# Kernel optimization log

Hardware: AMD Instinct MI355X
Metric: run time of the kernel (lower is better)

## Reference

```python
import jax, jax.numpy as jnp
import numpy as np

TOP_K = 128
HID = 256


def _mlp2(h, w1, b1, w2, b2):
    return jax.nn.relu(h @ w1 + b1) @ w2 + b2


def setup_inputs() -> dict:
    key = jax.random.key(0)
    ks = jax.random.split(key, 20)
    B, L, D = 512, 256, 64
    s = 0.05
    inp = {
        "x": jax.random.normal(ks[0], (B, L, D), dtype=jnp.float32),
        "Wq": jax.random.normal(ks[1], (D, HID)) * s, "bq": jnp.zeros((HID,)),
        "Wk": jax.random.normal(ks[2], (D, HID)) * s, "bk": jnp.zeros((HID,)),
        "phi_w1": jax.random.normal(ks[3], (D, HID)) * s, "phi_b1": jnp.zeros((HID,)),
        "phi_w2": jax.random.normal(ks[4], (HID, HID)) * s, "phi_b2": jnp.zeros((HID,)),
        "xi_w1": jax.random.normal(ks[5], (2 * D, HID)) * s, "xi_b1": jnp.zeros((HID,)),
        "xi_w2": jax.random.normal(ks[6], (HID, HID)) * s, "xi_b2": jnp.zeros((HID,)),
        "rho_w1": jax.random.normal(ks[7], (HID, HID)) * s, "rho_b1": jnp.zeros((HID,)),
        "rho_w2": jax.random.normal(ks[8], (HID, 128)) * s, "rho_b2": jnp.zeros((128,)),
    }
    return inp


def reference(x, Wq, bq, Wk, bk, phi_w1, phi_b1, phi_w2, phi_b2,
              xi_w1, xi_b1, xi_w2, xi_b2, rho_w1, rho_b1, rho_w2, rho_b2):
    B, L, D = x.shape
    scale = HID ** (-0.5)
    # padding mask (all True for randn input; trim is identity with static shapes)
    pad = jnp.sum(jnp.abs(x), axis=-1) != 0  # [B, L]
    Q = x @ Wq + bq  # [B, L, H]
    K = x @ Wk + bk
    scores = jnp.einsum("blh,bmh->blm", Q, K) * scale  # [B, L, L]
    mask2d = pad[:, :, None] & pad[:, None, :]
    scores = jnp.where(mask2d, scores, -jnp.inf)
    flat = scores.reshape(B, L * L)
    k = min(TOP_K, L * L)
    topk_vals, topk_idx = jax.lax.top_k(flat, k)  # [B, k]
    topk_w = jax.nn.softmax(topk_vals, axis=-1)
    row = topk_idx // L
    col = topk_idx % L
    x_i = jnp.take_along_axis(x, row[:, :, None], axis=1)  # [B, k, D]
    x_j = jnp.take_along_axis(x, col[:, :, None], axis=1)
    feat_self = _mlp2(x_i, phi_w1, phi_b1, phi_w2, phi_b2)  # [B, k, H]
    feat_pair = _mlp2(jnp.concatenate([x_i, x_j], axis=-1), xi_w1, xi_b1, xi_w2, xi_b2)
    self_mask = (row == col)[:, :, None]
    interaction = jnp.where(self_mask, feat_self, feat_pair)
    pooled = jnp.sum(interaction * topk_w[:, :, None], axis=1)  # [B, H]
    return _mlp2(pooled, rho_w1, rho_b1, rho_w2, rho_b2)  # [B, 128]
```

## Files before the change

### kernel.cpp

```cpp
#include <hip/hip_runtime.h>

typedef unsigned short u16;
typedef unsigned int   u32;
typedef unsigned char  u8;
typedef unsigned long long u64;

#define B_TOT 512
#define L_SEQ 256
#define D_IN  64
#define HIDN  256
#define TOPK  128
#define CAP   160
#define NWT   32
#define FLDS  76304

typedef float  f32x4  __attribute__((ext_vector_type(4)));
typedef __bf16 bf16x8 __attribute__((ext_vector_type(8)));

__device__ __forceinline__ u16 f2bf(float f){
  u32 u = __float_as_uint(f);
  u32 r = u + 0x7fffu + ((u>>16)&1u);
  return (u16)(r>>16);
}
__device__ __forceinline__ u32 sortKey(float f){
  u32 b = __float_as_uint(f);
  return (b & 0x80000000u) ? ~b : (b | 0x80000000u);
}
__device__ __forceinline__ float unKey(u32 u){
  u32 b = (u & 0x80000000u) ? (u & 0x7fffffffu) : ~u;
  return __uint_as_float(b);
}
__device__ __forceinline__ void cvt8(const float* v, u32* hp, u32* lp){
  #pragma unroll
  for (int i=0;i<4;++i){
    float v0 = v[2*i], v1 = v[2*i+1];
    u16 h0 = f2bf(v0); float h0f = __uint_as_float(((u32)h0)<<16); u16 l0 = f2bf(v0 - h0f);
    u16 h1 = f2bf(v1); float h1f = __uint_as_float(((u32)h1)<<16); u16 l1 = f2bf(v1 - h1f);
    hp[i] = (u32)h0 | ((u32)h1<<16);
    lp[i] = (u32)l0 | ((u32)l1<<16);
  }
}

__global__ __launch_bounds__(256) void k_wprep(
    const float* __restrict__ Wq, const float* __restrict__ bq,
    const float* __restrict__ Wk, const float* __restrict__ bk,
    const float* __restrict__ xi_w1, const float* __restrict__ phi_w1,
    u16* __restrict__ MtH, u16* __restrict__ MtL, float* __restrict__ uvc,
    u16* __restrict__ xiH, u16* __restrict__ xiL,
    u16* __restrict__ phiH, u16* __restrict__ phiL)
{
  int bid = blockIdx.x, tid = threadIdx.x;
  if (bid < 64){
    __shared__ float wq[HIDN];
    __shared__ float part[256];
    int a = bid;
    wq[tid] = Wq[a*HIDN + tid];
    __syncthreads();
    int bcol = tid & 63, q = tid >> 6;
    float s = 0.f;
    for (int h = q*64; h < q*64 + 64; ++h)
      s = fmaf(wq[h], Wk[bcol*HIDN + h], s);
    part[tid] = s;
    __syncthreads();
    if (tid < 64){
      float mv = part[tid] + part[64+tid] + part[128+tid] + part[192+tid];
      u16 hh = f2bf(mv); float hf = __uint_as_float(((u32)hh)<<16);
      u16 ll = f2bf(mv - hf);
      MtH[tid*64 + a] = hh;
      MtL[tid*64 + a] = ll;
    }
    int wv = tid >> 6, ln = tid & 63;
    if (wv == 0){
      float s2 = 0.f;
      #pragma unroll
      for (int i=0;i<4;++i){ int h = ln*4+i; s2 = fmaf(wq[h], bk[h], s2); }
      #pragma unroll
      for (int off=1; off<64; off<<=1) s2 += __shfl_xor(s2, off);
      if (ln == 0) uvc[a] = s2;
    } else if (wv == 1){
      float s2 = 0.f;
      #pragma unroll
      for (int i=0;i<4;++i){ int h = ln*4+i; s2 = fmaf(Wk[a*HIDN + h], bq[h], s2); }
      #pragma unroll
      for (int off=1; off<64; off<<=1) s2 += __shfl_xor(s2, off);
      if (ln == 0) uvc[64 + a] = s2;
    } else if (wv == 2 && a == 0){
      float s2 = 0.f;
      #pragma unroll
      for (int i=0;i<4;++i){ int h = ln*4+i; s2 = fmaf(bq[h], bk[h], s2); }
      #pragma unroll
      for (int off=1; off<64; off<<=1) s2 += __shfl_xor(s2, off);
      if (ln == 0) uvc[128] = s2;
    }
  } else {
    int t = (bid-64)*256 + tid;
    if (t < 256*128){
      int h = t >> 7, d = t & 127;
      float v = xi_w1[d*HIDN + h];
      u16 hh = f2bf(v); float hf = __uint_as_float(((u32)hh)<<16);
      u16 ll = f2bf(v - hf);
      xiH[h*128 + d] = hh; xiL[h*128 + d] = ll;
    } else {
      int t2 = t - 256*128;
      int h = t2 >> 6, d = t2 & 63;
      float v = phi_w1[d*HIDN + h];
      u16 hh = f2bf(v); float hf = __uint_as_float(((u32)hh)<<16);
      u16 ll = f2bf(v - hf);
      phiH[h*64 + d] = hh; phiL[h*64 + d] = ll;
    }
  }
}

__global__ __launch_bounds__(1024, 1) void k_fused(
    const float* __restrict__ x, const u16* __restrict__ MtH, const u16* __restrict__ MtL,
    const float* __restrict__ uvc,
    u64* __restrict__ cand, int* __restrict__ cand_n, u32* __restrict__ uthr)
{
  extern __shared__ __align__(16) u16 smem[];
  u16* XH = smem;
  u16* XL = XH + 256*72;
  float* STS = (float*)(XL + 256*72);
  float* STT = STS + 256;
  float* SUV = STT + 256;

  int tid = threadIdx.x;
  int b = blockIdx.x;
  const float* xb = x + (size_t)b*(L_SEQ*D_IN);

  if (tid < 129) SUV[tid] = uvc[tid];

  int ar = tid >> 2, aq = tid & 3;
  float v[16];
  {
    const float* src = xb + (size_t)ar*D_IN + aq*16;
    #pragma unroll
    for (int i=0;i<4;++i) *(float4*)&v[i*4] = *(const float4*)(src + i*4);
    u32 hpA[4],lpA[4],hpB[4],lpB[4];
    cvt8(&v[0], hpA, lpA); cvt8(&v[8], hpB, lpB);
    u16* dh = XH + ar*72 + aq*16;
    u16* dl = XL + ar*72 + aq*16;
    *(uint4*)(dh)     = make_uint4(hpA[0],hpA[1],hpA[2],hpA[3]);
    *(uint4*)(dh + 8) = make_uint4(hpB[0],hpB[1],hpB[2],hpB[3]);
    *(uint4*)(dl)     = make_uint4(lpA[0],lpA[1],lpA[2],lpA[3]);
    *(uint4*)(dl + 8) = make_uint4(lpB[0],lpB[1],lpB[2],lpB[3]);
  }
  __syncthreads();

  {
    float su=0.f, tv=0.f, pa=0.f;
    #pragma unroll
    for (int d=0; d<16; ++d){
      float xa = v[d];
      su = fmaf(xa, SUV[aq*16+d], su);
      tv = fmaf(xa, SUV[64+aq*16+d], tv);
      pa += fabsf(xa);
    }
    su += __shfl_xor(su,1); su += __shfl_xor(su,2);
    tv += __shfl_xor(tv,1); tv += __shfl_xor(tv,2);
    pa += __shfl_xor(pa,1); pa += __shfl_xor(pa,2);
    if (aq == 0){
      bool pad = (pa != 0.f);
      STS[ar] = pad ? (su + SUV[128]) : -1e38f;
      STT[ar] = pad ? tv : -1e38f;
    }
  }
  __syncthreads();

  int w = tid >> 6, lane = tid & 63, lm = lane & 15, quad = lane >> 4;
  int u  = w;
  int r0 = u*16;

  bf16x8 Yh0, Yh1, Yl0, Yl1;
  {
    const u16* xh_ = XH + (r0+lm)*72;
    const u16* xl_ = XL + (r0+lm)*72;
    bf16x8 Xh0 = *(const bf16x8*)(xh_ + quad*8);
    bf16x8 Xh1 = *(const bf16x8*)(xh_ + 32 + quad*8);
    bf16x8 Xl0 = *(const bf16x8*)(xl_ + quad*8);
    bf16x8 Xl1 = *(const bf16x8*)(xl_ + 32 + quad*8);
    u32 yh[8], yl[8];
    #pragma unroll
    for (int ct=0; ct<4; ++ct){
      int srow = 8*(lm>>2) + 4*(ct&1) + (lm&3) + 32*(ct>>1);
      const u16* mth = MtH + srow*64 + quad*8;
      const u16* mtl = MtL + srow*64 + quad*8;
      bf16x8 Mh0 = *(const bf16x8*)(mth);
      bf16x8 Mh1 = *(const bf16x8*)(mth + 32);
      bf16x8 Ml0 = *(const bf16x8*)(mtl);
      bf16x8 Ml1 = *(const bf16x8*)(mtl + 32);
      f32x4 a1 = {0.f,0.f,0.f,0.f}, a2 = {0.f,0.f,0.f,0.f};
      a1 = __builtin_amdgcn_mfma_f32_16x16x32_bf16(Mh0, Xh0, a1, 0,0,0);
      a2 = __builtin_amdgcn_mfma_f32_16x16x32_bf16(Mh1, Xh1, a2, 0,0,0);
      a1 = __builtin_amdgcn_mfma_f32_16x16x32_bf16(Ml0, Xh0, a1, 0,0,0);
      a2 = __builtin_amdgcn_mfma_f32_16x16x32_bf16(Ml1, Xh1, a2, 0,0,0);
      a1 = __builtin_amdgcn_mfma_f32_16x16x32_bf16(Mh0, Xl0, a1, 0,0,0);
      a2 = __builtin_amdgcn_mfma_f32_16x16x32_bf16(Mh1, Xl1, a2, 0,0,0);
      #pragma unroll
      for (int pr=0; pr<2; ++pr){
        float v0 = a1[2*pr]   + a2[2*pr];
        float v1 = a1[2*pr+1] + a2[2*pr+1];
        u16 h0 = f2bf(v0); u16 h1 = f2bf(v1);
        u16 l0 = f2bf(v0 - __uint_as_float(((u32)h0)<<16));
        u16 l1 = f2bf(v1 - __uint_as_float(((u32)h1)<<16));
        int slot = (ct>>1)*4 + (ct&1)*2 + pr;
        yh[slot] = (u32)h0 | ((u32)h1<<16);
        yl[slot] = (u32)l0 | ((u32)l1<<16);
      }
    }
    uint4 t0 = make_uint4(yh[0],yh[1],yh[2],yh[3]);
    uint4 t1 = make_uint4(yh[4],yh[5],yh[6],yh[7]);
    uint4 t2 = make_uint4(yl[0],yl[1],yl[2],yl[3]);
    uint4 t3 = make_uint4(yl[4],yl[5],yl[6],yl[7]);
    Yh0 = *(const bf16x8*)&t0;
    Yh1 = *(const bf16x8*)&t1;
    Yl0 = *(const bf16x8*)&t2;
    Yl1 = *(const bf16x8*)&t3;
  }

  float sr[4];
  #pragma unroll
  for (int r=0;r<4;++r) sr[r] = STS[r0 + quad*4 + r];

  for (int ch=0; ch<2; ++ch){
    int j0 = ch*128;
    u32 kv[32];
    #pragma unroll
    for (int ct=0; ct<8; ++ct){
      const u16* bh = XH + (j0 + ct*16+lm)*72;
      const u16* bl = XL + (j0 + ct*16+lm)*72;
      bf16x8 Bh0 = *(const bf16x8*)(bh + quad*8);
      bf16x8 Bh1 = *(const bf16x8*)(bh + 32 + quad*8);
      bf16x8 Bl0 = *(const bf16x8*)(bl + quad*8);
      bf16x8 Bl1 = *(const bf16x8*)(bl + 32 + quad*8);
      f32x4 a1 = {0.f,0.f,0.f,0.f}, a2 = {0.f,0.f,0.f,0.f};
      a1 = __builtin_amdgcn_mfma_f32_16x16x32_bf16(Yh0, Bh0, a1, 0,0,0);
      a2 = __builtin_amdgcn_mfma_f32_16x16x32_bf16(Yh1, Bh1, a2, 0,0,0);
      a1 = __builtin_amdgcn_mfma_f32_16x16x32_bf16(Yl0, Bh0, a1, 0,0,0);
      a2 = __builtin_amdgcn_mfma_f32_16x16x32_bf16(Yl1, Bh1, a2, 0,0,0);
      a1 = __builtin_amdgcn_mfma_f32_16x16x32_bf16(Yh0, Bl0, a1, 0,0,0);
      a2 = __builtin_amdgcn_mfma_f32_16x16x32_bf16(Yh1, Bl1, a2, 0,0,0);
      float tc = STT[j0 + ct*16 + lm];
      #pragma unroll
      for (int r=0;r<4;++r)
        kv[ct*4 + r] = sortKey(a1[r] + a2[r] + sr[r] + tc);
    }

    u32 T = 0;
    for (int bit=15; bit>=0; --bit){
      u32 th2 = (T | (1u<<bit)) << 16;
      int c0 = 0, c1 = 0;
      #pragma unroll
      for (int i=0;i<32;i+=2){
        c0 += (int)__popcll(__ballot(kv[i]   >= th2));
        c1 += (int)__popcll(__ballot(kv[i+1] >= th2));
      }
      int c = c0 + c1;
      if (c >= TOPK){
        T |= (1u<<bit);
        if (c <= CAP) break;
      }
    }
    u32 thr = T << 16;
    u32 up  = (T < 0xffffu) ? ((T+1u) << 16) : 0xffffffffu;

    u32 m1 = 0, m2 = 0;
    #pragma unroll
    for (int i=0;i<32;++i){
      bool ge = kv[i] >= thr;
      bool c1 = ge && (kv[i] >= up);
      m1 |= (c1 ? 1u : 0u) << i;
      m2 |= ((ge && !c1) ? 1u : 0u) << i;
    }
    int n1 = __popc(m1), n2 = __popc(m2);
    int p1 = n1, p2 = n2;
    #pragma unroll
    for (int off=1; off<64; off<<=1){
      int a = __shfl_up(p1, off); if (lane >= off) p1 += a;
      int c = __shfl_up(p2, off); if (lane >= off) p2 += c;
    }
    int tot1 = __shfl(p1, 63), tot2 = __shfl(p2, 63);
    int pos1 = p1 - n1;
    int pos2 = tot1 + (p2 - n2);
    int total = tot1 + tot2;
    int wt = u*2 + ch;
    size_t base = ((size_t)b*NWT + wt)*CAP;
    if (lane == 0){
      cand_n[b*NWT + wt] = (total < CAP) ? total : CAP;
      uthr[b*NWT + wt] = thr;
    }
    {
      int o1=0, o2=0;
      #pragma unroll
      for (int i=0;i<32;++i){
        bool c1 = (m1 >> i) & 1u, c2v = (m2 >> i) & 1u;
        if (c1 | c2v){
          int p = c1 ? (pos1 + o1) : (pos2 + o2);
          int flat = (r0 + quad*4 + (i&3))*L_SEQ + (j0 + (i>>2)*16 + lm);
          if (p < CAP) cand[base + p] = ((u64)kv[i] << 32) | (u32)flat;
        }
        o1 += c1; o2 += c2v;
      }
    }
  }
}

__global__ __launch_bounds__(256) void k_pre(
    const float* __restrict__ x, const u16* __restrict__ MtH, const u16* __restrict__ MtL,
    const float* __restrict__ uvc,
    u16* __restrict__ xh, u16* __restrict__ xl,
    u16* __restrict__ yh, u16* __restrict__ yl,
    float* __restrict__ st)
{
  __shared__ __align__(16) u16 sh[64][72];
  __shared__ __align__(16) u16 sl[64][72];
  __shared__ float sUV[132];
  int tid = threadIdx.x;
  int g0 = blockIdx.x * 64;
  int b  = g0 >> 8, l0 = g0 & 255;
  int r = tid >> 2, q = tid & 3;

  if (tid < 129) sUV[tid] = uvc[tid];

  float v[16];
  {
    const float* xr = x + (size_t)(g0 + r)*D_IN + q*16;
    #pragma unroll
    for (int i=0;i<4;++i) *(float4*)&v[i*4] = *(const float4*)(xr + i*4);
  }
  {
    u32 hpA[4],lpA[4],hpB[4],lpB[4];
    cvt8(&v[0], hpA, lpA); cvt8(&v[8], hpB, lpB);
    size_t xo = (size_t)(g0 + r)*D_IN + q*16;
    *(uint4*)(xh + xo)     = make_uint4(hpA[0],hpA[1],hpA[2],hpA[3]);
    *(uint4*)(xh + xo + 8) = make_uint4(hpB[0],hpB[1],hpB[2],hpB[3]);
    *(uint4*)(xl + xo)     = make_uint4(lpA[0],lpA[1],lpA[2],lpA[3]);
    *(uint4*)(xl + xo + 8) = make_uint4(lpB[0],lpB[1],lpB[2],lpB[3]);
    *(uint4*)&sh[r][q*16]   = make_uint4(hpA[0],hpA[1],hpA[2],hpA[3]);
    *(uint4*)&sh[r][q*16+8] = make_uint4(hpB[0],hpB[1],hpB[2],hpB[3]);
    *(uint4*)&sl[r][q*16]   = make_uint4(lpA[0],lpA[1],lpA[2],lpA[3]);
    *(uint4*)&sl[r][q*16+8] = make_uint4(lpB[0],lpB[1],lpB[2],lpB[3]);
  }
  __syncthreads();

  {
    float su=0.f, tv=0.f, pa=0.f;
    #pragma unroll
    for (int d=0; d<16; ++d){
      float xa = v[d];
      su = fmaf(xa, sUV[q*16+d], su);
      tv = fmaf(xa, sUV[64+q*16+d], tv);
      pa += fabsf(xa);
    }
    su += __shfl_xor(su,1); su += __shfl_xor(su,2);
    tv += __shfl_xor(tv,1); tv += __shfl_xor(tv,2);
    pa += __shfl_xor(pa,1); pa += __shfl_xor(pa,2);
    if (q == 0){
      bool pad = (pa != 0.f);
      st[(size_t)b*L_SEQ + l0 + r]          = pad ? (su + sUV[128]) : -1e38f;
      st[(size_t)(B_TOT+b)*L_SEQ + l0 + r]  = pad ? tv : -1e38f;
    }
  }

  int w = tid >> 6, lane = tid & 63, lm = lane & 15, quad = lane >> 4;
  bf16x8 Ah0 = *(const bf16x8*)&sh[w*16+lm][quad*8];
  bf16x8 Ah1 = *(const bf16x8*)&sh[w*16+lm][32 + quad*8];
  bf16x8 Al0 = *(const bf16x8*)&sl[w*16+lm][quad*8];
  bf16x8 Al1 = *(const bf16x8*)&sl[w*16+lm][32 + quad*8];
  #pragma unroll
  for (int ct=0; ct<4; ++ct){
    const u16* mth = MtH + (ct*16+lm)*64 + quad*8;
    const u16* mtl = MtL + (ct*16+lm)*64 + quad*8;
    bf16x8 Bh0 = *(const bf16x8*)(mth);
    bf16x8 Bh1 = *(const bf16x8*)(mth + 32);
    bf16x8 Bl0 = *(const bf16x8*)(mtl);
    bf16x8 Bl1 = *(const bf16x8*)(mtl + 32);
    f32x4 a1 = {0.f,0.f,0.f,0.f}, a2 = {0.f,0.f,0.f,0.f};
    a1 = __builtin_amdgcn_mfma_f32_16x16x32_bf16(Ah0, Bh0, a1, 0,0,0);
    a2 = __builtin_amdgcn_mfma_f32_16x16x32_bf16(Ah1, Bh1, a2, 0,0,0);
    a1 = __builtin_amdgcn_mfma_f32_16x16x32_bf16(Al0, Bh0, a1, 0,0,0);
    a2 = __builtin_amdgcn_mfma_f32_16x16x32_bf16(Al1, Bh1, a2, 0,0,0);
    a1 = __builtin_amdgcn_mfma_f32_16x16x32_bf16(Ah0, Bl0, a1, 0,0,0);
    a2 = __builtin_amdgcn_mfma_f32_16x16x32_bf16(Ah1, Bl1, a2, 0,0,0);
    #pragma unroll
    for (int rg=0; rg<4; ++rg){
      float vy = a1[rg] + a2[rg];
      u16 hh = f2bf(vy); float hf = __uint_as_float(((u32)hh)<<16);
      u16 ll = f2bf(vy - hf);
      sh[w*16 + quad*4 + rg][ct*16 + lm] = hh;
      sl[w*16 + quad*4 + rg][ct*16 + lm] = ll;
    }
  }
  {
    size_t yo = (size_t)(g0 + r)*D_IN + q*16;
    *(uint4*)(yh + yo)     = *(uint4*)&sh[r][q*16];
    *(uint4*)(yh + yo + 8) = *(uint4*)&sh[r][q*16+8];
    *(uint4*)(yl + yo)     = *(uint4*)&sl[r][q*16];
    *(uint4*)(yl + yo + 8) = *(uint4*)&sl[r][q*16+8];
  }
}

__global__ __launch_bounds__(256) void k_score(
    const u16* __restrict__ xh, const u16* __restrict__ xl,
    const u16* __restrict__ yh, const u16* __restrict__ yl,
    const float* __restrict__ st,
    u64* __restrict__ cand, int* __restrict__ cand_n, u32* __restrict__ uthr)
{
  int tid = threadIdx.x;
  int lin = blockIdx.x;
  int b    = ((lin >> 6) << 3) | (lin & 7);
  int tile = (lin >> 3) & 7;
  int cb = tile & 1, rb = tile >> 1;
  int r0 = rb*64, j0 = cb*128;
  int w = tid >> 6, lane = tid & 63, lm = lane & 15, quad = lane >> 4;

  size_t rowA = ((size_t)b*L_SEQ + r0 + w*16 + lm)*D_IN;
  bf16x8 A_h0 = *(const bf16x8*)(yh + rowA + quad*8);
  bf16x8 A_h1 = *(const bf16x8*)(yh + rowA + 32 + quad*8);
  bf16x8 A_l0 = *(const bf16x8*)(yl + rowA + quad*8);
  bf16x8 A_l1 = *(const bf16x8*)(yl + rowA + 32 + quad*8);

  float4 s4 = *(const float4*)(st + (size_t)b*L_SEQ + r0 + w*16 + quad*4);
  float sr[4] = {s4.x, s4.y, s4.z, s4.w};
  float tc[8];
  #pragma unroll
  for (int ct=0;ct<8;++ct)
    tc[ct] = st[(size_t)(B_TOT + b)*L_SEQ + j0 + ct*16 + lm];

  u32 kv[32];
  #pragma unroll
  for (int ct=0; ct<8; ++ct){
    size_t rowB = ((size_t)b*L_SEQ + j0 + ct*16 + lm)*D_IN;
    bf16x8 B_h0 = *(const bf16x8*)(xh + rowB + quad*8);
    bf16x8 B_h1 = *(const bf16x8*)(xh + rowB + 32 + quad*8);
    bf16x8 B_l0 = *(const bf16x8*)(xl + rowB + quad*8);
    bf16x8 B_l1 = *(const bf16x8*)(xl + rowB + 32 + quad*8);
    f32x4 a1 = {0.f,0.f,0.f,0.f}, a2 = {0.f,0.f,0.f,0.f};
    a1 = __builtin_amdgcn_mfma_f32_16x16x32_bf16(A_h0, B_h0, a1, 0,0,0);
    a2 = __builtin_amdgcn_mfma_f32_16x16x32_bf16(A_h1, B_h1, a2, 0,0,0);
    a1 = __builtin_amdgcn_mfma_f32_16x16x32_bf16(A_l0, B_h0, a1, 0,0,0);
    a2 = __builtin_amdgcn_mfma_f32_16x16x32_bf16(A_l1, B_h1, a2, 0,0,0);
    a1 = __builtin_amdgcn_mfma_f32_16x16x32_bf16(A_h0, B_l0, a1, 0,0,0);
    a2 = __builtin_amdgcn_mfma_f32_16x16x32_bf16(A_h1, B_l1, a2, 0,0,0);
    #pragma unroll
    for (int r=0;r<4;++r)
      kv[ct*4 + r] = sortKey(a1[r] + a2[r] + sr[r] + tc[ct]);
  }

  u32 T = 0;
  for (int bit=15; bit>=0; --bit){
    u32 th2 = (T | (1u<<bit)) << 16;
    int c = 0;
    #pragma unroll
    for (int i=0;i<32;++i)
      c += (int)__popcll(__ballot(kv[i] >= th2));
    if (c >= TOPK){
      T |= (1u<<bit);
      if (c <= CAP) break;
    }
  }
  u32 thr = T << 16;

  u32 hm = 0;
  #pragma unroll
  for (int i=0;i<32;++i) hm |= (kv[i] >= thr ? 1u : 0u) << i;
  int myc = __popc(hm);
  int pre = myc;
  #pragma unroll
  for (int off=1; off<64; off<<=1){
    int n = __shfl_up(pre, off);
    if (lane >= off) pre += n;
  }
  int total = __shfl(pre, 63);
  int pos = pre - myc;
  int wt = tile*4 + w;
  size_t base = ((size_t)b*NWT + wt)*CAP;
  if (lane == 0){
    cand_n[b*NWT + wt] = (total < CAP) ? total : CAP;
    uthr[b*NWT + wt] = thr;
  }
  while (hm){
    int i = __ffs(hm) - 1; hm &= hm - 1;
    if (pos < CAP){
      int r = i & 3, ct = i >> 2;
      int flat = (r0 + w*16 + quad*4 + r)*L_SEQ + (j0 + ct*16 + lm);
      cand[base + pos] = ((u64)kv[i] << 32) | (u32)flat;
    }
    ++pos;
  }
}

__global__ __launch_bounds__(256) void k_merge(
    const u64* __restrict__ cand, const int* __restrict__ cand_n, const u32* __restrict__ uthr,
    int* __restrict__ selidx, float* __restrict__ selw)
{
  const int SL   = NWT/4;
  const int NSW  = SL*CAP/64;
  const int WCAP = 192;
  __shared__ u64 wbuf[4][WCAP];
  __shared__ int wcnt[4];
  __shared__ int scnt[NWT];
  __shared__ u32 wT[4];
  __shared__ int cm, eqc;
  __shared__ int eqi[256];
  __shared__ float sv[TOPK]; __shared__ int si[TOPK];
  __shared__ float fred[8];
  int b = blockIdx.x, tid = threadIdx.x;
  int w = tid >> 6, lane = tid & 63;
  if (tid < NWT) scnt[tid] = cand_n[b*NWT + tid];
  if (tid == 0){ cm = 0; eqc = 0; }
  __syncthreads();

  u32 key[NSW]; int idx[NSW];
  size_t bb = (size_t)b*NWT*CAP + (size_t)(w*SL)*CAP;
  #pragma unroll
  for (int s=0;s<NSW;++s){
    int e = lane + 64*s;
    int slot = e / CAP, p = e - slot*CAP;
    bool ok = p < scnt[w*SL + slot];
    u64 v = ok ? cand[bb + e] : 0ull;
    key[s] = (u32)(v >> 32);
    idx[s] = ok ? (int)(u32)v : 0x7fffffff;
  }

  u32 lb = uthr[b*NWT + w*SL + (lane & 7)];
  #pragma unroll
  for (int off=1; off<8; off<<=1){
    u32 o = (u32)__shfl_xor((int)lb, off);
    lb = lb > o ? lb : o;
  }

  u32 T = 0;
  for (int bit=31; bit>=0; --bit){
    u32 c2 = T | (1u<<bit);
    if (c2 <= lb){ T = c2; continue; }
    int c = 0;
    #pragma unroll
    for (int s=0;s<NSW;++s) c += (int)__popcll(__ballot(key[s] >= c2));
    if (c >= TOPK){
      T = c2;
      if (c <= WCAP) break;
    }
  }
  if (lane == 0) wT[w] = T;
  {
    int myc = 0;
    #pragma unroll
    for (int s=0;s<NSW;++s) myc += (key[s] >= T) ? 1 : 0;
    int pre = myc;
    #pragma unroll
    for (int off=1; off<64; off<<=1){
      int n = __shfl_up(pre, off);
      if (lane >= off) pre += n;
    }
    int total = __shfl(pre, 63);
    int pos = pre - myc;
    if (lane == 0) wcnt[w] = (total < WCAP) ? total : WCAP;
    #pragma unroll
    for (int s=0;s<NSW;++s){
      if (key[s] >= T){
        if (pos < WCAP) wbuf[w][pos] = ((u64)key[s] << 32) | (u32)idx[s];
        ++pos;
      }
    }
  }
  __syncthreads();

  if (w == 0){
    const int NS2 = 4*WCAP/64;
    u32 k2[NS2]; int i2[NS2];
    #pragma unroll
    for (int s=0;s<NS2;++s){
      int e = lane + 64*s;
      int slot = e / WCAP, p = e - slot*WCAP;
      bool ok = p < wcnt[slot];
      u64 v = ok ? wbuf[slot][p] : 0ull;
      k2[s] = (u32)(v >> 32);
      i2[s] = ok ? (int)(u32)v : 0x7fffffff;
    }
    u32 lb2 = wT[0];
    lb2 = lb2 > wT[1] ? lb2 : wT[1];
    lb2 = lb2 > wT[2] ? lb2 : wT[2];
    lb2 = lb2 > wT[3] ? lb2 : wT[3];
    u32 T2 = 0;
    for (int bit=31; bit>=0; --bit){
      u32 c2 = T2 | (1u<<bit);
      if (c2 <= lb2){ T2 = c2; continue; }
      int c = 0;
      #pragma unroll
      for (int s=0;s<NS2;++s) c += (int)__popcll(__ballot(k2[s] >= c2));
      if (c >= TOPK) T2 = c2;
    }
    int m = 0;
    #pragma unroll
    for (int s=0;s<NS2;++s) m += (int)__popcll(__ballot(k2[s] > T2));
    #pragma unroll
    for (int s=0;s<NS2;++s){
      if (k2[s] > T2){
        int p = atomicAdd(&cm, 1);
        sv[p] = unKey(k2[s]) * 0.0625f; si[p] = i2[s];
      } else if (k2[s] == T2 && i2[s] != 0x7fffffff){
        int q = atomicAdd(&eqc, 1);
        if (q < 256) eqi[q] = i2[s];
      }
    }
    if (lane == 0){
      int need = TOPK - m;
      int n = eqc < 256 ? eqc : 256;
      float tv = unKey(T2) * 0.0625f;
      for (int s2=0; s2<need; ++s2){
        int bi = s2;
        for (int j=s2+1;j<n;++j) if (eqi[j] < eqi[bi]) bi = j;
        int t2 = eqi[s2]; eqi[s2] = eqi[bi]; eqi[bi] = t2;
        sv[m+s2] = tv; si[m+s2] = eqi[s2];
      }
    }
  }
  __syncthreads();

  float v = (tid < TOPK) ? sv[tid] : -3.4e38f;
  float mx = v;
  #pragma unroll
  for (int off=1; off<64; off<<=1) mx = fmaxf(mx, __shfl_xor(mx, off));
  if ((tid&63)==0) fred[tid>>6] = mx;
  __syncthreads();
  mx = fmaxf(fred[0], fred[1]);
  float e = (tid < TOPK) ? expf(v - mx) : 0.f;
  float s = e;
  #pragma unroll
  for (int off=1; off<64; off<<=1) s += __shfl_xor(s, off);
  if ((tid&63)==0) fred[4 + (tid>>6)] = s;
  __syncthreads();
  s = fred[4] + fred[5];
  if (tid < TOPK){
    selw[(size_t)b*TOPK + tid]   = e / s;
    selidx[(size_t)b*TOPK + tid] = si[tid];
  }
}

__global__ __launch_bounds__(256) void k_mlp(
    const float* __restrict__ x, const int* __restrict__ selidx, const float* __restrict__ selw,
    const u16* __restrict__ xiH, const u16* __restrict__ xiL,
    const u16* __restrict__ phiH, const u16* __restrict__ phiL,
    const float* __restrict__ phi_b1, const float* __restrict__ phi_w2, const float* __restrict__ phi_b2,
    const float* __restrict__ xi_b1,  const float* __restrict__ xi_w2,  const float* __restrict__ xi_b2,
    const float* __restrict__ rho_w1, const float* __restrict__ rho_b1,
    const float* __restrict__ rho_w2, const float* __restrict__ rho_b2,
    float* __restrict__ out)
{
  __shared__ __align__(16) u16 AFh[8][4][64][8];
  __shared__ __align__(16) u16 AFl[8][4][64][8];
  __shared__ int   sidx[TOPK];
  __shared__ float swp[TOPK], swd[TOPK];
  __shared__ float gpL[256], gsL[256];
  __shared__ float pooled[256], t1[256];
  __shared__ float wsums[2];
  int b = blockIdx.x, tid = threadIdx.x;

  if (tid < TOPK){
    int fl = selidx[(size_t)b*TOPK + tid];
    sidx[tid] = fl;
    float wv = selw[(size_t)b*TOPK + tid];
    bool dg = ((fl>>8) == (fl&255));
    swp[tid] = dg ? 0.f : wv;
    swd[tid] = dg ? wv  : 0.f;
  }
  __syncthreads();
  if (tid == 0){
    float a=0.f, c2=0.f;
    for (int k=0;k<TOPK;++k){ a+=swp[k]; c2+=swd[k]; }
    wsums[0]=a; wsums[1]=c2;
  }
  {
    int m = tid >> 1, hf = tid & 1;
    int fl = sidx[m];
    int rc = hf ? (fl & 255) : (fl >> 8);
    const float* src = x + ((size_t)b*L_SEQ + rc)*D_IN;
    int kt = m >> 4, l16 = m & 15;
    #pragma unroll
    for (int g=0; g<8; ++g){
      int d0 = hf*64 + g*8;
      int c = d0 >> 5, q = (d0 >> 3) & 3;
      float v[8];
      *(float4*)&v[0] = *(const float4*)(src + (d0 & 63));
      *(float4*)&v[4] = *(const float4*)(src + (d0 & 63) + 4);
      u32 hp[4], lp[4];
      cvt8(v, hp, lp);
      *(uint4*)&AFh[kt][c][l16 + 16*q][0] = make_uint4(hp[0],hp[1],hp[2],hp[3]);
      *(uint4*)&AFl[kt][c][l16 + 16*q][0] = make_uint4(lp[0],lp[1],lp[2],lp[3]);
    }
  }
  __syncthreads();

  int w = tid >> 6, lane = tid & 63;
  int lm = lane & 15, quad = lane >> 4;

  #pragma unroll
  for (int hi4=0; hi4<4; ++hi4){
    int ht = w + 4*hi4;
    int h  = ht*16 + lm;
    bf16x8 BXh[4], BXl[4], BPh[2], BPl[2];
    #pragma unroll
    for (int c=0;c<4;++c){
      BXh[c] = *(const bf16x8*)(xiH + h*128 + c*32 + quad*8);
      BXl[c] = *(const bf16x8*)(xiL + h*128 + c*32 + quad*8);
    }
    #pragma unroll
    for (int c=0;c<2;++c){
      BPh[c] = *(const bf16x8*)(phiH + h*64 + c*32 + quad*8);
      BPl[c] = *(const bf16x8*)(phiL + h*64 + c*32 + quad*8);
    }
    float bxi = xi_b1[h], bph = phi_b1[h];
    float gp = 0.f, gs = 0.f;
    for (int kt=0; kt<8; ++kt){
      bf16x8 Ah_[4], Al_[4];
      #pragma unroll
      for (int c=0;c<4;++c){
        Ah_[c] = *(const bf16x8*)&AFh[kt][c][lane][0];
        Al_[c] = *(const bf16x8*)&AFl[kt][c][lane][0];
      }
      f32x4 cx = {0.f,0.f,0.f,0.f}, cp = {0.f,0.f,0.f,0.f};
      #pragma unroll
      for (int c=0;c<4;++c){
        cx = __builtin_amdgcn_mfma_f32_16x16x32_bf16(Ah_[c], BXh[c], cx, 0,0,0);
        cx = __builtin_amdgcn_mfma_f32_16x16x32_bf16(Al_[c], BXh[c], cx, 0,0,0);
        cx = __builtin_amdgcn_mfma_f32_16x16x32_bf16(Ah_[c], BXl[c], cx, 0,0,0);
      }
      #pragma unroll
      for (int c=0;c<2;++c){
        cp = __builtin_amdgcn_mfma_f32_16x16x32_bf16(Ah_[c], BPh[c], cp, 0,0,0);
        cp = __builtin_amdgcn_mfma_f32_16x16x32_bf16(Al_[c], BPh[c], cp, 0,0,0);
        cp = __builtin_amdgcn_mfma_f32_16x16x32_bf16(Ah_[c], BPl[c], cp, 0,0,0);
      }
      #pragma unroll
      for (int r=0;r<4;++r){
        int kk = kt*16 + quad*4 + r;
        gp = fmaf(swp[kk], fmaxf(cx[r] + bxi, 0.f), gp);
        gs = fmaf(swd[kk], fmaxf(cp[r] + bph, 0.f), gs);
      }
    }
    gp += __shfl_xor(gp, 16); gp += __shfl_xor(gp, 32);
    gs += __shfl_xor(gs, 16); gs += __shfl_xor(gs, 32);
    if (quad == 0){ gpL[h] = gp; gsL[h] = gs; }
  }
  __syncthreads();

  int h = tid;
  {
    float wsp = wsums[0], wss = wsums[1];
    float po = wsp*xi_b2[h] + wss*phi_b2[h];
    for (int d=0; d<256; ++d){
      po = fmaf(gpL[d], xi_w2[d*HIDN + h], po);
      po = fmaf(gsL[d], phi_w2[d*HIDN + h], po);
    }
    pooled[h] = po;
  }
  __syncthreads();
  {
    float a = rho_b1[h];
    for (int d=0; d<256; ++d) a = fmaf(pooled[d], rho_w1[d*HIDN + h], a);
    t1[h] = fmaxf(a, 0.f);
  }
  __syncthreads();
  if (h < 128){
    float o = rho_b2[h];
    for (int d=0; d<256; ++d) o = fmaf(t1[d], rho_w2[d*128 + h], o);
    out[(size_t)b*128 + h] = o;
  }
}

extern "C" void kernel_launch(void* const* d_in, const int* in_sizes, int n_in,
                              void* d_out, int out_size, void* d_ws, size_t ws_size,
                              hipStream_t stream)
{
  (void)in_sizes; (void)n_in; (void)out_size; (void)ws_size;
  const float* x      = (const float*)d_in[0];
  const float* Wq     = (const float*)d_in[1];
  const float* bq     = (const float*)d_in[2];
  const float* Wk     = (const float*)d_in[3];
  const float* bk     = (const float*)d_in[4];
  const float* phi_w1 = (const float*)d_in[5];
  const float* phi_b1 = (const float*)d_in[6];
  const float* phi_w2 = (const float*)d_in[7];
  const float* phi_b2 = (const float*)d_in[8];
  const float* xi_w1  = (const float*)d_in[9];
  const float* xi_b1  = (const float*)d_in[10];
  const float* xi_w2  = (const float*)d_in[11];
  const float* xi_b2  = (const float*)d_in[12];
  const float* rho_w1 = (const float*)d_in[13];
  const float* rho_b1 = (const float*)d_in[14];
  const float* rho_w2 = (const float*)d_in[15];
  const float* rho_b2 = (const float*)d_in[16];
  float* out = (float*)d_out;

  const size_t NX = (size_t)B_TOT*L_SEQ*D_IN;
  float* uvc    = (float*)d_ws;
  float* st     = uvc + 256;
  float* selw   = st + (size_t)2*B_TOT*L_SEQ;
  int*   selidx = (int*)(selw + (size_t)B_TOT*TOPK);
  int*   cand_n = selidx + (size_t)B_TOT*TOPK;
  u32*   uthr   = (u32*)(cand_n + (size_t)B_TOT*NWT);
  u64*   cand   = (u64*)(uthr + (size_t)B_TOT*NWT);
  u16*   MtH    = (u16*)(cand + (size_t)B_TOT*NWT*CAP);
  u16*   MtL    = MtH + 64*64;
  u16*   xiH    = MtL + 64*64;
  u16*   xiL    = xiH + 256*128;
  u16*   phiH   = xiL + 256*128;
  u16*   phiL   = phiH + 256*64;
  u16*   xh     = phiL + 256*64;
  u16*   xl     = xh + NX;
  u16*   yh     = xl + NX;
  u16*   yl     = yh + NX;

  hipError_t aerr = hipFuncSetAttribute((const void*)k_fused,
                      hipFuncAttributeMaxDynamicSharedMemorySize, FLDS);

  k_wprep<<<dim3(256),  dim3(256), 0, stream>>>(Wq, bq, Wk, bk, xi_w1, phi_w1,
                                                MtH, MtL, uvc, xiH, xiL, phiH, phiL);
  if (aerr == hipSuccess){
    k_fused<<<dim3(B_TOT), dim3(1024), FLDS, stream>>>(x, MtH, MtL, uvc, cand, cand_n, uthr);
  } else {
    k_pre  <<<dim3(2048), dim3(256), 0, stream>>>(x, MtH, MtL, uvc, xh, xl, yh, yl, st);
    k_score<<<dim3(4096), dim3(256), 0, stream>>>(xh, xl, yh, yl, st, cand, cand_n, uthr);
  }
  k_merge<<<dim3(B_TOT), dim3(256), 0, stream>>>(cand, cand_n, uthr, selidx, selw);
  k_mlp  <<<dim3(B_TOT), dim3(256), 0, stream>>>(x, selidx, selw,
            xiH, xiL, phiH, phiL,
            phi_b1, phi_w2, phi_b2,
            xi_b1, xi_w2, xi_b2,
            rho_w1, rho_b1, rho_w2, rho_b2, out);
}
```

Measured before the change: 255.5 us.

## Fuse top-k candidate merge and softmax into the scoring kernel via shared memory

```diff
diff --git a/kernel.cpp b/kernel.cpp
--- a/kernel.cpp
+++ b/kernel.cpp
@@ -12,7 +12,7 @@
 #define TOPK  128
 #define CAP   160
 #define NWT   32
-#define FLDS  76304
+#define FLDS  113984
 
 typedef float  f32x4  __attribute__((ext_vector_type(4)));
 typedef __bf16 bf16x8 __attribute__((ext_vector_type(8)));
@@ -114,20 +114,34 @@
 __global__ __launch_bounds__(1024, 1) void k_fused(
     const float* __restrict__ x, const u16* __restrict__ MtH, const u16* __restrict__ MtL,
     const float* __restrict__ uvc,
-    u64* __restrict__ cand, int* __restrict__ cand_n, u32* __restrict__ uthr)
+    int* __restrict__ selidx, float* __restrict__ selw)
 {
   extern __shared__ __align__(16) u16 smem[];
   u16* XH = smem;
   u16* XL = XH + 256*72;
-  float* STS = (float*)(XL + 256*72);
-  float* STT = STS + 256;
-  float* SUV = STT + 256;
+  float* STS  = (float*)(XL + 256*72);
+  float* STT  = STS + 256;
+  float* SUV  = STT + 256;
+  u32*  candK = (u32*)(SUV + 129);
+  u32*  wTT   = candK + NWT*CAP;
+  int*  wcn   = (int*)(wTT + 16);
+  u32*  gbK   = (u32*)(wcn + 16);
+  u32*  gTT   = gbK + 4*192;
+  int*  gcn   = (int*)(gTT + 4);
+  float* sv   = (float*)(gcn + 4);
+  int*  si    = (int*)(sv + 128);
+  float* fred = (float*)(si + 128);
+  int*  cmx   = (int*)(fred + 32);
+  int*  eqi   = cmx + 2;
+  u16*  candI = (u16*)(eqi + 256);
+  u16*  gbI   = candI + NWT*CAP;
 
   int tid = threadIdx.x;
   int b = blockIdx.x;
   const float* xb = x + (size_t)b*(L_SEQ*D_IN);
 
   if (tid < 129) SUV[tid] = uvc[tid];
+  if (tid == 0){ cmx[0] = 0; cmx[1] = 0; }
 
   int ar = tid >> 2, aq = tid & 3;
   float v[16];
@@ -221,6 +235,8 @@
   #pragma unroll
   for (int r=0;r<4;++r) sr[r] = STS[r0 + quad*4 + r];
 
+  int cn0 = 0, cn1 = 0;
+  u32 th0 = 0, th1 = 0;
   for (int ch=0; ch<2; ++ch){
     int j0 = ch*128;
     u32 kv[32];
@@ -283,11 +299,9 @@
     int pos2 = tot1 + (p2 - n2);
     int total = tot1 + tot2;
     int wt = u*2 + ch;
-    size_t base = ((size_t)b*NWT + wt)*CAP;
-    if (lane == 0){
-      cand_n[b*NWT + wt] = (total < CAP) ? total : CAP;
-      uthr[b*NWT + wt] = thr;
-    }
+    int cbase = wt*CAP;
+    if (ch == 0){ cn0 = (total < CAP) ? total : CAP; th0 = thr; }
+    else        { cn1 = (total < CAP) ? total : CAP; th1 = thr; }
     {
       int o1=0, o2=0;
       #pragma unroll
@@ -296,10 +310,178 @@
         if (c1 | c2v){
           int p = c1 ? (pos1 + o1) : (pos2 + o2);
           int flat = (r0 + quad*4 + (i&3))*L_SEQ + (j0 + (i>>2)*16 + lm);
-          if (p < CAP) cand[base + p] = ((u64)kv[i] << 32) | (u32)flat;
+          if (p < CAP){ candK[cbase + p] = kv[i]; candI[cbase + p] = (u16)flat; }
         }
         o1 += c1; o2 += c2v;
       }
+    }
+  }
+
+  const int WCAP = 192;
+
+  {
+    u32 k1[5]; u16 i1[5];
+    #pragma unroll
+    for (int s=0;s<5;++s){
+      int e = lane + 64*s;
+      int slot = (e >= CAP) ? 1 : 0;
+      int p = e - slot*CAP;
+      int cc = slot ? cn1 : cn0;
+      bool ok = p < cc;
+      int base2 = (u*2+slot)*CAP;
+      k1[s] = ok ? candK[base2+p] : 0u;
+      i1[s] = ok ? candI[base2+p] : (u16)0;
+    }
+    u32 lb = th0 > th1 ? th0 : th1;
+    u32 T = 0;
+    for (int bit=31; bit>=0; --bit){
+      u32 c2 = T | (1u<<bit);
+      if (c2 <= lb){ T = c2; continue; }
+      int c = 0;
+      #pragma unroll
+      for (int s=0;s<5;++s) c += (int)__popcll(__ballot(k1[s] >= c2));
+      if (c >= TOPK){ T = c2; if (c <= WCAP) break; }
+    }
+    int myc = 0;
+    #pragma unroll
+    for (int s=0;s<5;++s) myc += (k1[s] >= T) ? 1 : 0;
+    int pre = myc;
+    #pragma unroll
+    for (int off=1; off<64; off<<=1){
+      int n = __shfl_up(pre, off);
+      if (lane >= off) pre += n;
+    }
+    int total = __shfl(pre, 63);
+    int pos = pre - myc;
+    if (lane == 0){ wcn[w] = (total < WCAP) ? total : WCAP; wTT[w] = T; }
+    u32* wbK = candK + w*(2*CAP);
+    u16* wbI = candI + w*(2*CAP);
+    #pragma unroll
+    for (int s=0;s<5;++s){
+      if (k1[s] >= T){
+        if (pos < WCAP){ wbK[pos] = k1[s]; wbI[pos] = i1[s]; }
+        ++pos;
+      }
+    }
+  }
+  __syncthreads();
+
+  if (w < 4){
+    u32 k2[12]; u16 i2[12];
+    #pragma unroll
+    for (int s=0;s<12;++s){
+      int e = lane + 64*s;
+      int slot = e / WCAP, p = e - slot*WCAP;
+      int sw = w*4 + slot;
+      bool ok = p < wcn[sw];
+      k2[s] = ok ? candK[sw*(2*CAP)+p] : 0u;
+      i2[s] = ok ? candI[sw*(2*CAP)+p] : (u16)0;
+    }
+    u32 lb = wTT[w*4];
+    #pragma unroll
+    for (int t=1;t<4;++t){ u32 o = wTT[w*4+t]; lb = lb > o ? lb : o; }
+    u32 T = 0;
+    for (int bit=31; bit>=0; --bit){
+      u32 c2 = T | (1u<<bit);
+      if (c2 <= lb){ T = c2; continue; }
+      int c = 0;
+      #pragma unroll
+      for (int s=0;s<12;++s) c += (int)__popcll(__ballot(k2[s] >= c2));
+      if (c >= TOPK){ T = c2; if (c <= WCAP) break; }
+    }
+    int myc = 0;
+    #pragma unroll
+    for (int s=0;s<12;++s) myc += (k2[s] >= T) ? 1 : 0;
+    int pre = myc;
+    #pragma unroll
+    for (int off=1; off<64; off<<=1){
+      int n = __shfl_up(pre, off);
+      if (lane >= off) pre += n;
+    }
+    int total = __shfl(pre, 63);
+    int pos = pre - myc;
+    if (lane == 0){ gcn[w] = (total < WCAP) ? total : WCAP; gTT[w] = T; }
+    #pragma unroll
+    for (int s=0;s<12;++s){
+      if (k2[s] >= T){
+        if (pos < WCAP){ gbK[w*WCAP + pos] = k2[s]; gbI[w*WCAP + pos] = i2[s]; }
+        ++pos;
+      }
+    }
+  }
+  __syncthreads();
+
+  if (w == 0){
+    u32 k3[12]; u16 i3[12];
+    #pragma unroll
+    for (int s=0;s<12;++s){
+      int e = lane + 64*s;
+      int slot = e / WCAP, p = e - slot*WCAP;
+      bool ok = p < gcn[slot];
+      k3[s] = ok ? gbK[slot*WCAP+p] : 0u;
+      i3[s] = ok ? gbI[slot*WCAP+p] : (u16)0;
+    }
+    u32 lb = gTT[0];
+    #pragma unroll
+    for (int t=1;t<4;++t){ u32 o = gTT[t]; lb = lb > o ? lb : o; }
+    u32 T3 = 0;
+    for (int bit=31; bit>=0; --bit){
+      u32 c2 = T3 | (1u<<bit);
+      if (c2 <= lb){ T3 = c2; continue; }
+      int c = 0;
+      #pragma unroll
+      for (int s=0;s<12;++s) c += (int)__popcll(__ballot(k3[s] >= c2));
+      if (c >= TOPK) T3 = c2;
+    }
+    int m = 0;
+    #pragma unroll
+    for (int s=0;s<12;++s) m += (int)__popcll(__ballot(k3[s] > T3));
+    #pragma unroll
+    for (int s=0;s<12;++s){
+      if (k3[s] > T3){
+        int p = atomicAdd(&cmx[0], 1);
+        sv[p] = unKey(k3[s]) * 0.0625f; si[p] = (int)i3[s];
+      } else if (k3[s] == T3 && k3[s] != 0u){
+        int q = atomicAdd(&cmx[1], 1);
+        if (q < 256) eqi[q] = (int)i3[s];
+      }
+    }
+    if (lane == 0){
+      int need = TOPK - m;
+      int n = cmx[1] < 256 ? cmx[1] : 256;
+      float tv = unKey(T3) * 0.0625f;
+      for (int s2=0; s2<need; ++s2){
+        int bi = s2;
+        for (int j=s2+1;j<n;++j) if (eqi[j] < eqi[bi]) bi = j;
+        int t2 = eqi[s2]; eqi[s2] = eqi[bi]; eqi[bi] = t2;
+        sv[m+s2] = tv; si[m+s2] = eqi[s2];
+      }
+    }
+  }
+  __syncthreads();
+
+  {
+    float vv = (tid < TOPK) ? sv[tid] : -3.4e38f;
+    float mx = vv;
+    #pragma unroll
+    for (int off=1; off<64; off<<=1) mx = fmaxf(mx, __shfl_xor(mx, off));
+    if (lane == 0) fred[w] = mx;
+    __syncthreads();
+    mx = fred[0];
+    #pragma unroll
+    for (int t=1;t<16;++t) mx = fmaxf(mx, fred[t]);
+    float e = (tid < TOPK) ? expf(vv - mx) : 0.f;
+    float sum = e;
+    #pragma unroll
+    for (int off=1; off<64; off<<=1) sum += __shfl_xor(sum, off);
+    if (lane == 0) fred[16 + w] = sum;
+    __syncthreads();
+    float s = 0.f;
+    #pragma unroll
+    for (int t=0;t<16;++t) s += fred[16+t];
+    if (tid < TOPK){
+      selw[(size_t)b*TOPK + tid]   = e / s;
+      selidx[(size_t)b*TOPK + tid] = si[tid];
     }
   }
 }
@@ -817,12 +999,12 @@
   k_wprep<<<dim3(256),  dim3(256), 0, stream>>>(Wq, bq, Wk, bk, xi_w1, phi_w1,
                                                 MtH, MtL, uvc, xiH, xiL, phiH, phiL);
   if (aerr == hipSuccess){
-    k_fused<<<dim3(B_TOT), dim3(1024), FLDS, stream>>>(x, MtH, MtL, uvc, cand, cand_n, uthr);
+    k_fused<<<dim3(B_TOT), dim3(1024), FLDS, stream>>>(x, MtH, MtL, uvc, selidx, selw);
   } else {
     k_pre  <<<dim3(2048), dim3(256), 0, stream>>>(x, MtH, MtL, uvc, xh, xl, yh, yl, st);
     k_score<<<dim3(4096), dim3(256), 0, stream>>>(xh, xl, yh, yl, st, cand, cand_n, uthr);
-  }
-  k_merge<<<dim3(B_TOT), dim3(256), 0, stream>>>(cand, cand_n, uthr, selidx, selw);
+    k_merge<<<dim3(B_TOT), dim3(256), 0, stream>>>(cand, cand_n, uthr, selidx, selw);
+  }
   k_mlp  <<<dim3(B_TOT), dim3(256), 0, stream>>>(x, selidx, selw,
             xiH, xiL, phiH, phiL,
             phi_b1, phi_w2, phi_b2,
```

Result: slower. 265.3 us (+3.8%).

## Widen k_mlp to 512 threads with split-K dense layers and wave reductions

Applied to the files above, without the earlier changes.

```diff
diff --git a/kernel.cpp b/kernel.cpp
--- a/kernel.cpp
+++ b/kernel.cpp
@@ -111,7 +111,7 @@
   }
 }
 
-__global__ __launch_bounds__(1024, 1) void k_fused(
+__global__ void __launch_bounds__(1024) __attribute__((amdgpu_waves_per_eu(4))) k_fused(
     const float* __restrict__ x, const u16* __restrict__ MtH, const u16* __restrict__ MtL,
     const float* __restrict__ uvc,
     u64* __restrict__ cand, int* __restrict__ cand_n, u32* __restrict__ uthr)
@@ -637,7 +637,7 @@
   }
 }
 
-__global__ __launch_bounds__(256) void k_mlp(
+__global__ __launch_bounds__(512) void k_mlp(
     const float* __restrict__ x, const int* __restrict__ selidx, const float* __restrict__ selw,
     const u16* __restrict__ xiH, const u16* __restrict__ xiL,
     const u16* __restrict__ phiH, const u16* __restrict__ phiL,
@@ -653,8 +653,10 @@
   __shared__ float swp[TOPK], swd[TOPK];
   __shared__ float gpL[256], gsL[256];
   __shared__ float pooled[256], t1[256];
+  __shared__ float pp[512];
   __shared__ float wsums[2];
   int b = blockIdx.x, tid = threadIdx.x;
+  int w = tid >> 6, lane = tid & 63;
 
   if (tid < TOPK){
     int fl = selidx[(size_t)b*TOPK + tid];
@@ -665,38 +667,43 @@
     swd[tid] = dg ? wv  : 0.f;
   }
   __syncthreads();
-  if (tid == 0){
-    float a=0.f, c2=0.f;
-    for (int k=0;k<TOPK;++k){ a+=swp[k]; c2+=swd[k]; }
-    wsums[0]=a; wsums[1]=c2;
-  }
-  {
-    int m = tid >> 1, hf = tid & 1;
+
+  if (w == 0){
+    float a = swp[lane] + swp[64 + lane];
+    #pragma unroll
+    for (int off=1; off<64; off<<=1) a += __shfl_xor(a, off);
+    if (lane == 0) wsums[0] = a;
+  } else if (w == 1){
+    float a = swd[lane] + swd[64 + lane];
+    #pragma unroll
+    for (int off=1; off<64; off<<=1) a += __shfl_xor(a, off);
+    if (lane == 0) wsums[1] = a;
+  }
+
+  {
+    int m = tid >> 2, qq = tid & 3;
     int fl = sidx[m];
-    int rc = hf ? (fl & 255) : (fl >> 8);
-    const float* src = x + ((size_t)b*L_SEQ + rc)*D_IN;
+    int rc = (qq < 2) ? (fl >> 8) : (fl & 255);
+    const float* src = x + ((size_t)b*L_SEQ + rc)*D_IN + (qq & 1)*32;
     int kt = m >> 4, l16 = m & 15;
     #pragma unroll
-    for (int g=0; g<8; ++g){
-      int d0 = hf*64 + g*8;
-      int c = d0 >> 5, q = (d0 >> 3) & 3;
+    for (int g=0; g<4; ++g){
       float v[8];
-      *(float4*)&v[0] = *(const float4*)(src + (d0 & 63));
-      *(float4*)&v[4] = *(const float4*)(src + (d0 & 63) + 4);
+      *(float4*)&v[0] = *(const float4*)(src + g*8);
+      *(float4*)&v[4] = *(const float4*)(src + g*8 + 4);
       u32 hp[4], lp[4];
       cvt8(v, hp, lp);
-      *(uint4*)&AFh[kt][c][l16 + 16*q][0] = make_uint4(hp[0],hp[1],hp[2],hp[3]);
-      *(uint4*)&AFl[kt][c][l16 + 16*q][0] = make_uint4(lp[0],lp[1],lp[2],lp[3]);
-    }
-  }
-  __syncthreads();
-
-  int w = tid >> 6, lane = tid & 63;
+      *(uint4*)&AFh[kt][qq][l16 + 16*g][0] = make_uint4(hp[0],hp[1],hp[2],hp[3]);
+      *(uint4*)&AFl[kt][qq][l16 + 16*g][0] = make_uint4(lp[0],lp[1],lp[2],lp[3]);
+    }
+  }
+  __syncthreads();
+
   int lm = lane & 15, quad = lane >> 4;
 
   #pragma unroll
-  for (int hi4=0; hi4<4; ++hi4){
-    int ht = w + 4*hi4;
+  for (int hi2=0; hi2<2; ++hi2){
+    int ht = w + 8*hi2;
     int h  = ht*16 + lm;
     bf16x8 BXh[4], BXl[4], BPh[2], BPl[2];
     #pragma unroll
@@ -744,28 +751,40 @@
   }
   __syncthreads();
 
-  int h = tid;
-  {
+  {
+    int h = tid & 255, half = tid >> 8;
     float wsp = wsums[0], wss = wsums[1];
-    float po = wsp*xi_b2[h] + wss*phi_b2[h];
-    for (int d=0; d<256; ++d){
+    float po = (half == 0) ? (wsp*xi_b2[h] + wss*phi_b2[h]) : 0.f;
+    int dd0 = half*128;
+    for (int d=dd0; d<dd0+128; ++d){
       po = fmaf(gpL[d], xi_w2[d*HIDN + h], po);
       po = fmaf(gsL[d], phi_w2[d*HIDN + h], po);
     }
-    pooled[h] = po;
-  }
-  __syncthreads();
-  {
-    float a = rho_b1[h];
-    for (int d=0; d<256; ++d) a = fmaf(pooled[d], rho_w1[d*HIDN + h], a);
-    t1[h] = fmaxf(a, 0.f);
-  }
-  __syncthreads();
-  if (h < 128){
-    float o = rho_b2[h];
-    for (int d=0; d<256; ++d) o = fmaf(t1[d], rho_w2[d*128 + h], o);
-    out[(size_t)b*128 + h] = o;
-  }
+    pp[half*256 + h] = po;
+  }
+  __syncthreads();
+  if (tid < 256) pooled[tid] = pp[tid] + pp[256 + tid];
+  __syncthreads();
+  {
+    int h = tid & 255, half = tid >> 8;
+    float a = (half == 0) ? rho_b1[h] : 0.f;
+    int dd0 = half*128;
+    for (int d=dd0; d<dd0+128; ++d) a = fmaf(pooled[d], rho_w1[d*HIDN + h], a);
+    pp[half*256 + h] = a;
+  }
+  __syncthreads();
+  if (tid < 256) t1[tid] = fmaxf(pp[tid] + pp[256 + tid], 0.f);
+  __syncthreads();
+  {
+    int h = tid & 127, part = tid >> 7;
+    float o = (part == 0) ? rho_b2[h] : 0.f;
+    int dd0 = part*64;
+    for (int d=dd0; d<dd0+64; ++d) o = fmaf(t1[d], rho_w2[d*128 + h], o);
+    pp[part*128 + h] = o;
+  }
+  __syncthreads();
+  if (tid < 128)
+    out[(size_t)b*128 + tid] = pp[tid] + pp[128+tid] + pp[256+tid] + pp[384+tid];
 }
 
 extern "C" void kernel_launch(void* const* d_in, const int* in_sizes, int n_in,
@@ -823,7 +842,7 @@
     k_score<<<dim3(4096), dim3(256), 0, stream>>>(xh, xl, yh, yl, st, cand, cand_n, uthr);
   }
   k_merge<<<dim3(B_TOT), dim3(256), 0, stream>>>(cand, cand_n, uthr, selidx, selw);
-  k_mlp  <<<dim3(B_TOT), dim3(256), 0, stream>>>(x, selidx, selw,
+  k_mlp  <<<dim3(B_TOT), dim3(512), 0, stream>>>(x, selidx, selw,
             xiH, xiL, phiH, phiL,
             phi_b1, phi_w2, phi_b2,
             xi_b1, xi_w2, xi_b2,
```

After: 250.6 us. Within noise of the previous version (-1.9%).
